# Optimization experiments

Hardware: AMD Instinct MI355X
Metric: run time of the kernel (lower is better)

## Reference

```python
import jax, jax.numpy as jnp
import numpy as np

NEG_SLOPE = 0.2
NUM_NODES = 100000
NUM_EDGES = 200000
NNZ = 1600000
IN_C = 128
OUT_C = 128
STAR = 64


def setup_inputs() -> dict:
    key = jax.random.key(0)
    ks = jax.random.split(key, 12)
    X = jax.random.normal(ks[0], (NUM_NODES, IN_C), dtype=jnp.float32)
    V = jax.random.randint(ks[1], (NNZ,), 0, NUM_NODES)
    E = jax.random.randint(ks[2], (NNZ,), 0, NUM_EDGES)
    S_features = jax.random.normal(ks[3], (NUM_EDGES, STAR), dtype=jnp.float32)
    s = 1.0 / np.sqrt(IN_C)
    Wx = jax.random.uniform(ks[4], (IN_C, OUT_C), minval=-s, maxval=s)
    bx = jax.random.uniform(ks[5], (OUT_C,), minval=-s, maxval=s)
    Wv = jax.random.uniform(ks[6], (IN_C, OUT_C), minval=-s, maxval=s)
    bv = jax.random.uniform(ks[7], (OUT_C,), minval=-s, maxval=s)
    sa = 1.0 / np.sqrt(OUT_C)
    a_vec = jax.random.uniform(ks[8], (OUT_C,), minval=-sa, maxval=sa)
    st = 1.0 / np.sqrt(OUT_C + STAR)
    Wt = jax.random.uniform(ks[9], (OUT_C + STAR, OUT_C), minval=-st, maxval=st)
    bt = jax.random.uniform(ks[10], (OUT_C,), minval=-st, maxval=st)
    return {"X": X, "V": V, "E": E, "S_features": S_features,
            "Wx": Wx, "bx": bx, "Wv": Wv, "bv": bv,
            "a_vec": a_vec, "Wt": Wt, "bt": bt}


def _segment_softmax(s, seg, num_segments):
    m = jax.ops.segment_max(s, seg, num_segments=num_segments)
    e = jnp.exp(s - m[seg])
    denom = jax.ops.segment_sum(e, seg, num_segments=num_segments)
    return e / denom[seg]


def reference(X, V, E, S_features, Wx, bx, Wv, bv, a_vec, Wt, bt):
    # DPHGNNConv forward (eval mode: dropout = identity)
    X_init = X @ Wx + bx                      # [N, out]
    X_feat = X @ Wv + bv                      # [N, out]
    scores = X_feat @ a_vec                   # [N]
    s = jax.nn.leaky_relu(scores[V], NEG_SLOPE)  # [nnz]
    w = _segment_softmax(s, E, NUM_EDGES)     # [nnz]
    Xev = X_feat[V] * w[:, None]              # [nnz, out]
    Y_v2e = jax.ops.segment_sum(Xev, E, num_segments=NUM_EDGES)
    Y_v2e = jax.nn.elu(Y_v2e)
    e_msg = jnp.concatenate([Y_v2e, S_features], axis=1)  # [E, out+star]
    Y = e_msg @ Wt + bt                       # [E, out]
    Yev = Y[E]                                # [nnz, out]
    num = jax.ops.segment_sum(Yev, V, num_segments=NUM_NODES)
    cnt = jax.ops.segment_sum(jnp.ones((NNZ,), jnp.float32), V, num_segments=NUM_NODES)
    Xn = num / jnp.maximum(cnt, 1.0)[:, None]  # scatter_mean
    Xn = jax.nn.elu(Xn)                        # is_last=False
    return Xn + X_init
```

## Files before the change

kernel.cpp:

```cpp
#include <hip/hip_runtime.h>
#include <math.h>

#define N_NODES 100000
#define N_EDGES 200000
#define NNZ_    1600000
#define INC  128
#define OUTC 128
#define STAR_ 64
#define NEG 0.2f
#define NBIN_E 391
#define NBIN_V 196
#define NBIN (NBIN_E + NBIN_V)
#define CHUNK 4000
#define NBLK_A (NNZ_/CHUNK)
#define CAP_E 5120
#define CAP_V 9216
#define PAIR_SZ (NBIN_E*CAP_E + NBIN_V*CAP_V)
#define CAPI 288
#define CAPN 288

typedef __attribute__((ext_vector_type(8))) short bf16x8_t;
typedef __attribute__((ext_vector_type(8))) unsigned short u16x8;
typedef __attribute__((ext_vector_type(4))) float f32x4_t;

__device__ __forceinline__ float leaky(float x){ return x > 0.f ? x : NEG*x; }
__device__ __forceinline__ float elu1(float x){ return x > 0.f ? x : __expf(x)-1.f; }
__device__ __forceinline__ unsigned short f2bf(float f){
  unsigned u = __float_as_uint(f);
  unsigned r = u + 0x7FFFu + ((u >> 16) & 1u);
  return (unsigned short)(r >> 16);
}
__device__ __forceinline__ float bf2f(unsigned short h){
  return __uint_as_float(((unsigned)h) << 16);
}
__device__ __forceinline__ int padBaseD(int bin){
  return bin < NBIN_E ? bin*CAP_E : NBIN_E*CAP_E + (bin-NBIN_E)*CAP_V;
}

__global__ void k_cvt(const float* __restrict__ Wx, const float* __restrict__ Wv,
                      const float* __restrict__ Wt,
                      unsigned short* __restrict__ WcatT, unsigned short* __restrict__ WtT,
                      int* __restrict__ binCur,
                      int2* __restrict__ vw, int* __restrict__ eIdxV){
  const int i = blockIdx.x*256 + threadIdx.x;
  if (i < 256*128){
    const int n = i >> 7, k = i & 127;
    const float v = (n < 128) ? Wx[k*128 + n] : Wv[k*128 + (n-128)];
    WcatT[n*128 + k] = f2bf(v);
  }
  const int j = i - 256*128;
  if (j >= 0 && j < 128*192){
    const int n = j / 192, k = j - n*192;
    WtT[n*192 + k] = f2bf(Wt[k*128 + n]);
  }
  if (blockIdx.x == 0){
    for (int p = threadIdx.x; p < NBIN; p += 256) binCur[p] = padBaseD(p);
    if (threadIdx.x < 16){ vw[NNZ_ + threadIdx.x] = make_int2(0, 0); eIdxV[NNZ_ + threadIdx.x] = 0; }
  }
}

__global__ __launch_bounds__(256) void k_front(
    const float* __restrict__ X, const unsigned short* __restrict__ WcatT,
    const float* __restrict__ bx, const float* __restrict__ bv,
    const float* __restrict__ av,
    float* __restrict__ Xinit, unsigned short* __restrict__ Xfb,
    float* __restrict__ scores,
    const int* __restrict__ V, const int* __restrict__ E,
    int* __restrict__ binCur, int2* __restrict__ pair){
  __shared__ int hA[NBIN];
  __shared__ int baseA[NBIN];
  __shared__ unsigned short xb[16][136];
  __shared__ float sc[16];
  const int tid = threadIdx.x;

  if (blockIdx.x < NBLK_A) {
    for (int p = tid; p < NBIN; p += 256) hA[p] = 0;
    __syncthreads();
    const int start = blockIdx.x*CHUNK, end = start + CHUNK;
    for (int i = start + tid; i < end; i += 256){
      atomicAdd(&hA[E[i] >> 9], 1);
      atomicAdd(&hA[NBIN_E + (V[i] >> 9)], 1);
    }
    __syncthreads();
    for (int p = tid; p < NBIN; p += 256)
      baseA[p] = hA[p] ? atomicAdd(&binCur[p], hA[p]) : 0;
    __syncthreads();
    for (int p = tid; p < NBIN; p += 256) hA[p] = 0;
    __syncthreads();
    for (int i = start + tid; i < end; i += 256){
      const int e = E[i], v = V[i];
      const int be = e >> 9, bv_ = NBIN_E + (v >> 9);
      const int se = baseA[be]  + atomicAdd(&hA[be],  1);
      const int sv = baseA[bv_] + atomicAdd(&hA[bv_], 1);
      pair[se] = make_int2(e, v);
      pair[sv] = make_int2(v, e);
    }
    return;
  }

  const int lane = tid & 63, w = tid >> 6;
  const int quad = lane >> 4, l16 = lane & 15;
  const int r0 = (blockIdx.x - NBLK_A) * 16;
  if (tid < 16) sc[tid] = 0.f;
  {
    const int r = tid >> 4;
    const int c0 = (tid & 15) * 8;
    const float4 a4 = *(const float4*)&X[(size_t)(r0+r)*INC + c0];
    const float4 b4 = *(const float4*)&X[(size_t)(r0+r)*INC + c0 + 4];
    bf16x8_t pk;
    pk[0]=(short)f2bf(a4.x); pk[1]=(short)f2bf(a4.y); pk[2]=(short)f2bf(a4.z); pk[3]=(short)f2bf(a4.w);
    pk[4]=(short)f2bf(b4.x); pk[5]=(short)f2bf(b4.y); pk[6]=(short)f2bf(b4.z); pk[7]=(short)f2bf(b4.w);
    *(bf16x8_t*)&xb[r][c0] = pk;
  }
  __syncthreads();
  f32x4_t acc[4] = {{0,0,0,0},{0,0,0,0},{0,0,0,0},{0,0,0,0}};
  const int n_base = w*64 + l16;
  for (int s = 0; s < 4; ++s){
    const bf16x8_t af = *(const bf16x8_t*)&xb[l16][s*32 + quad*8];
    #pragma unroll
    for (int nt = 0; nt < 4; ++nt){
      const int n = n_base + nt*16;
      const bf16x8_t bf = *(const bf16x8_t*)&WcatT[(size_t)n*128 + s*32 + quad*8];
      acc[nt] = __builtin_amdgcn_mfma_f32_16x16x32_bf16(af, bf, acc[nt], 0, 0, 0);
    }
  }
  float pr[4] = {0.f, 0.f, 0.f, 0.f};
  #pragma unroll
  for (int nt = 0; nt < 4; ++nt){
    const int n = n_base + nt*16;
    const float bias = (n < 128) ? bx[n] : bv[n-128];
    #pragma unroll
    for (int r = 0; r < 4; ++r){
      const int m = quad*4 + r;
      const float val = acc[nt][r] + bias;
      if (n < 128) Xinit[(size_t)(r0+m)*OUTC + n] = val;
      else {
        Xfb[(size_t)(r0+m)*OUTC + (n-128)] = f2bf(val);
        pr[r] += val * av[n-128];
      }
    }
  }
  if (w >= 2){
    #pragma unroll
    for (int r = 0; r < 4; ++r) atomicAdd(&sc[quad*4 + r], pr[r]);
  }
  __syncthreads();
  if (tid < 16) scores[r0 + tid] = sc[tid];
}

__global__ __launch_bounds__(512) void k_binBE(const int2* __restrict__ pair,
    const int* __restrict__ binCur, const float* __restrict__ scores,
    int2* __restrict__ vw, int* __restrict__ cntE, int* __restrict__ startsE,
    float* __restrict__ dens){
  __shared__ int h[512], sc0[512], sc1[512];
  __shared__ float dsh[512];
  const int bin = blockIdx.x;
  const int bucket0 = bin << 9;
  const int pstart = padBaseD(bin);
  const int n = binCur[bin] - pstart;
  const int tid = threadIdx.x;
  {
    int part = 0;
    for (int p = tid; p < bin; p += 512) part += binCur[p] - padBaseD(p);
    sc0[tid] = part;
    __syncthreads();
    for (int o = 256; o; o >>= 1){ if (tid < o) sc0[tid] += sc0[tid+o]; __syncthreads(); }
  }
  const int itemBase = sc0[0];
  __syncthreads();
  h[tid] = 0; dsh[tid] = 0.f;
  __syncthreads();
  for (int j = tid; j < n; j += 512) atomicAdd(&h[pair[pstart + j].x & 511], 1);
  __syncthreads();
  sc0[tid] = h[tid];
  __syncthreads();
  int* a = sc0; int* b = sc1;
  for (int o = 1; o < 512; o <<= 1){
    b[tid] = a[tid] + (tid >= o ? a[tid-o] : 0);
    __syncthreads();
    int* t = a; a = b; b = t;
  }
  {
    const int excl = a[tid] - h[tid];
    b[tid] = itemBase + excl;
    const int bucket = bucket0 + tid;
    if (bucket < N_EDGES){ cntE[bucket] = h[tid]; startsE[bucket] = itemBase + excl; }
  }
  __syncthreads();
  for (int j = tid; j < n; j += 512){
    const int2 kv = pair[pstart + j];
    const int slot = atomicAdd(&b[kv.x & 511], 1);
    const float ex = __expf(leaky(scores[kv.y]));
    vw[slot] = make_int2(kv.y, __float_as_int(ex));
    atomicAdd(&dsh[kv.x & 511], ex);
  }
  __syncthreads();
  if (bucket0 + tid < N_EDGES) dens[bucket0 + tid] = dsh[tid];
}

__global__ __launch_bounds__(256) void k_edgeV(
    const int* __restrict__ cntE, const int* __restrict__ startsE,
    const int2* __restrict__ vw, const float* __restrict__ dens,
    const unsigned short* __restrict__ Xfb,
    const float* __restrict__ S, const unsigned short* __restrict__ WtT,
    const float* __restrict__ bt, unsigned short* __restrict__ Ybf,
    const int2* __restrict__ pair, const int* __restrict__ binCur,
    int* __restrict__ eIdxV, int* __restrict__ cntV, int* __restrict__ startsV) {
  __shared__ __align__(16) char smem[(CAPI + 8)*8 + 16*200*2];
  const int tid = threadIdx.x;

  if (blockIdx.x < NBIN_V) {
    int* h   = (int*)smem;
    int* sc0 = h + 512;
    int* sc1 = sc0 + 512;
    const int nb = blockIdx.x;
    const int bin = NBIN_E + nb;
    const int bucket0 = nb << 9;
    const int pstart = padBaseD(bin);
    const int n = binCur[bin] - pstart;
    {
      int part = 0;
      for (int p = tid; p < bin; p += 256) part += binCur[p] - padBaseD(p);
      sc0[tid] = part;
      __syncthreads();
      for (int o = 128; o; o >>= 1){ if (tid < o) sc0[tid] += sc0[tid+o]; __syncthreads(); }
    }
    const int itemBase = sc0[0] - NNZ_;
    __syncthreads();
    for (int p = tid; p < 512; p += 256) h[p] = 0;
    __syncthreads();
    for (int j = tid; j < n; j += 256) atomicAdd(&h[pair[pstart + j].x & 511], 1);
    __syncthreads();
    for (int p = tid; p < 512; p += 256) sc0[p] = h[p];
    __syncthreads();
    int* a = sc0; int* b = sc1;
    for (int o = 1; o < 512; o <<= 1){
      for (int p = tid; p < 512; p += 256) b[p] = a[p] + (p >= o ? a[p-o] : 0);
      __syncthreads();
      int* t = a; a = b; b = t;
    }
    for (int p = tid; p < 512; p += 256){
      const int excl = a[p] - h[p];
      b[p] = itemBase + excl;
      const int bucket = bucket0 + p;
      if (bucket < N_NODES){ cntV[bucket] = h[p]; startsV[bucket] = itemBase + excl; }
    }
    __syncthreads();
    for (int j = tid; j < n; j += 256){
      const int2 kv = pair[pstart + j];
      const int slot = atomicAdd(&b[kv.x & 511], 1);
      eIdxV[slot] = kv.y;
    }
    return;
  }

  int2* inc = (int2*)smem;
  unsigned short (*msg)[200] = (unsigned short (*)[200])(smem + (CAPI + 8)*8);
  const int lane = tid & 63, w = tid >> 6;
  const int e0 = (blockIdx.x - NBIN_V) * 16;
  const int g16 = tid >> 4, s16 = tid & 15;

  const int st0 = startsE[e0];
  const int lim = startsE[e0 + 15] + cntE[e0 + 15] - st0;

  for (int i = tid; i < CAPI + 8; i += 256)
    inc[i] = (i < lim) ? vw[st0 + i] : make_int2(0, 0);

  {
    const float4 s4 = *(const float4*)&S[(size_t)(e0+g16)*STAR_ + s16*4];
    ushort4 pk; pk.x=f2bf(s4.x); pk.y=f2bf(s4.y); pk.z=f2bf(s4.z); pk.w=f2bf(s4.w);
    *(ushort4*)&msg[g16][128 + s16*4] = pk;
  }
  __syncthreads();

  const int e = e0 + g16;
  const int deg = cntE[e];
  const int lo  = startsE[e] - st0;
  const int c8 = s16 * 8;
  float ac[8] = {0.f,0.f,0.f,0.f,0.f,0.f,0.f,0.f};
  if (lo + deg <= CAPI) {
    for (int j = 0; j < deg; j += 8) {
      int2 pp[8];
      #pragma unroll
      for (int k = 0; k < 8; ++k) pp[k] = inc[lo + j + k];
      u16x8 xx[8];
      #pragma unroll
      for (int k = 0; k < 8; ++k)
        xx[k] = *(const u16x8*)&Xfb[(size_t)pp[k].x*OUTC + c8];
      #pragma unroll
      for (int k = 0; k < 8; ++k) {
        const float wgt = (j + k < deg) ? __int_as_float(pp[k].y) : 0.f;
        #pragma unroll
        for (int q = 0; q < 8; ++q) ac[q] += wgt * bf2f(xx[k][q]);
      }
    }
  } else {
    const int st = st0 + lo;
    for (int j = 0; j < deg; j += 8) {
      int2 pp[8];
      #pragma unroll
      for (int k = 0; k < 8; ++k) pp[k] = vw[st + j + k];
      u16x8 xx[8];
      #pragma unroll
      for (int k = 0; k < 8; ++k)
        xx[k] = *(const u16x8*)&Xfb[(size_t)pp[k].x*OUTC + c8];
      #pragma unroll
      for (int k = 0; k < 8; ++k) {
        const float wgt = (j + k < deg) ? __int_as_float(pp[k].y) : 0.f;
        #pragma unroll
        for (int q = 0; q < 8; ++q) ac[q] += wgt * bf2f(xx[k][q]);
      }
    }
  }
  {
    const float invd = deg > 0 ? 1.f/dens[e] : 0.f;
    u16x8 pk;
    #pragma unroll
    for (int q = 0; q < 8; ++q) pk[q] = f2bf(elu1(ac[q]*invd));
    *(u16x8*)&msg[g16][c8] = pk;
  }
  __syncthreads();

  const int quad = lane >> 4, l16 = lane & 15;
  f32x4_t acc0 = {0,0,0,0}, acc1 = {0,0,0,0};
  const int n0 = w * 32;
  for (int s = 0; s < 6; ++s) {
    const bf16x8_t af = *(const bf16x8_t*)&msg[l16][s*32 + quad*8];
    const bf16x8_t b0 = *(const bf16x8_t*)&WtT[(size_t)(n0 + l16)*192      + s*32 + quad*8];
    const bf16x8_t b1 = *(const bf16x8_t*)&WtT[(size_t)(n0 + 16 + l16)*192 + s*32 + quad*8];
    acc0 = __builtin_amdgcn_mfma_f32_16x16x32_bf16(af, b0, acc0, 0, 0, 0);
    acc1 = __builtin_amdgcn_mfma_f32_16x16x32_bf16(af, b1, acc1, 0, 0, 0);
  }
  const float bt0 = bt[n0 + l16], bt1 = bt[n0 + 16 + l16];
  #pragma unroll
  for (int r = 0; r < 4; ++r) {
    const int m = quad*4 + r;
    Ybf[(size_t)(e0+m)*OUTC + n0 + l16]      = f2bf(acc0[r] + bt0);
    Ybf[(size_t)(e0+m)*OUTC + n0 + 16 + l16] = f2bf(acc1[r] + bt1);
  }
}

__global__ __launch_bounds__(256) void k_node(
    const int* __restrict__ cntV, const int* __restrict__ startsV,
    const int* __restrict__ eIdxV,
    const unsigned short* __restrict__ Ybf, float* __restrict__ out) {
  __shared__ int elds[CAPN + 8];
  const int tid = threadIdx.x;
  const int sub = tid & 31, grp = tid >> 5;
  const int v0 = blockIdx.x * 8;

  const int st0 = startsV[v0];
  const int lim = startsV[v0 + 7] + cntV[v0 + 7] - st0;
  for (int i = tid; i < CAPN + 8; i += 256)
    elds[i] = (i < lim) ? eIdxV[st0 + i] : 0;
  __syncthreads();

  const int v = v0 + grp;
  const int c4 = sub * 4;
  const int deg = cntV[v];
  const int lo  = startsV[v] - st0;
  float a0=0.f, a1=0.f, a2=0.f, a3=0.f;
  if (lo + deg <= CAPN) {
    for (int j = 0; j < deg; j += 8) {
      int ee[8];
      #pragma unroll
      for (int k = 0; k < 8; ++k) ee[k] = elds[lo + j + k];
      ushort4 yy[8];
      #pragma unroll
      for (int k = 0; k < 8; ++k)
        yy[k] = *(const ushort4*)&Ybf[(size_t)ee[k]*OUTC + c4];
      #pragma unroll
      for (int k = 0; k < 8; ++k) {
        const float pz = (j + k < deg) ? 1.f : 0.f;
        a0 += pz * bf2f(yy[k].x); a1 += pz * bf2f(yy[k].y);
        a2 += pz * bf2f(yy[k].z); a3 += pz * bf2f(yy[k].w);
      }
    }
  } else {
    const int st = st0 + lo;
    for (int j = 0; j < deg; j += 8) {
      int ee[8];
      #pragma unroll
      for (int k = 0; k < 8; ++k) ee[k] = eIdxV[st + j + k];
      ushort4 yy[8];
      #pragma unroll
      for (int k = 0; k < 8; ++k)
        yy[k] = *(const ushort4*)&Ybf[(size_t)ee[k]*OUTC + c4];
      #pragma unroll
      for (int k = 0; k < 8; ++k) {
        const float pz = (j + k < deg) ? 1.f : 0.f;
        a0 += pz * bf2f(yy[k].x); a1 += pz * bf2f(yy[k].y);
        a2 += pz * bf2f(yy[k].z); a3 += pz * bf2f(yy[k].w);
      }
    }
  }
  const float invd = 1.f / fmaxf((float)deg, 1.f);
  float4 o = *(float4*)&out[(size_t)v*OUTC + c4];
  o.x = elu1(a0*invd) + o.x;
  o.y = elu1(a1*invd) + o.y;
  o.z = elu1(a2*invd) + o.z;
  o.w = elu1(a3*invd) + o.w;
  *(float4*)&out[(size_t)v*OUTC + c4] = o;
}

extern "C" void kernel_launch(void* const* d_in, const int* in_sizes, int n_in,
                              void* d_out, int out_size, void* d_ws, size_t ws_size,
                              hipStream_t stream) {
  const float* X  = (const float*)d_in[0];
  const int*   V  = (const int*)d_in[1];
  const int*   E  = (const int*)d_in[2];
  const float* S  = (const float*)d_in[3];
  const float* Wx = (const float*)d_in[4];
  const float* bx = (const float*)d_in[5];
  const float* Wv = (const float*)d_in[6];
  const float* bv = (const float*)d_in[7];
  const float* av = (const float*)d_in[8];
  const float* Wt = (const float*)d_in[9];
  const float* bt = (const float*)d_in[10];
  float* out = (float*)d_out;

  char* ws = (char*)d_ws;
  size_t off = 0;
  auto alloc = [&](size_t bytes) -> void* {
    off = (off + 255) & ~(size_t)255;
    void* p = ws + off; off += bytes; return p;
  };
  unsigned short* Xfb   = (unsigned short*)alloc((size_t)N_NODES*OUTC*2);
  unsigned short* Ybf   = (unsigned short*)alloc((size_t)N_EDGES*OUTC*2);
  float* scores = (float*)alloc((size_t)N_NODES*4);
  unsigned short* WcatT = (unsigned short*)alloc((size_t)256*128*2);
  unsigned short* WtT   = (unsigned short*)alloc((size_t)128*192*2);
  int2* pair   = (int2*)alloc((size_t)PAIR_SZ*8);
  int* binCur  = (int*)alloc((size_t)NBIN*4);
  int* cntE    = (int*)alloc((size_t)N_EDGES*4);
  int* cntV    = (int*)alloc((size_t)N_NODES*4);
  int* startsE = (int*)alloc((size_t)N_EDGES*4);
  int* startsV = (int*)alloc((size_t)N_NODES*4);
  int2* vw     = (int2*)alloc((size_t)(NNZ_+16)*8);
  int* eIdxV   = (int*)alloc((size_t)(NNZ_+16)*4);
  float* dens  = (float*)alloc((size_t)N_EDGES*4);

  k_cvt<<<(256*128 + 128*192 + 255)/256, 256, 0, stream>>>(Wx, Wv, Wt, WcatT, WtT,
                                                           binCur, vw, eIdxV);
  k_front<<<NBLK_A + N_NODES/16, 256, 0, stream>>>(X, WcatT, bx, bv, av, out, Xfb, scores,
                                                   V, E, binCur, pair);
  k_binBE<<<NBIN_E, 512, 0, stream>>>(pair, binCur, scores, vw, cntE, startsE, dens);
  k_edgeV<<<NBIN_V + N_EDGES/16, 256, 0, stream>>>(cntE, startsE, vw, dens, Xfb, S, WtT, bt, Ybf,
                                                   pair, binCur, eIdxV, cntV, startsV);
  k_node<<<N_NODES/8, 256, 0, stream>>>(cntV, startsV, eIdxV, Ybf, out);
}
```

Before: 470.0 us.

## Precompute exp scores per node and fold softmax denominator into edge gather

Computes exp(leaky(score)) once per node in the front kernel instead of once per incidence in the binning kernel. The binning kernel now writes only vertex indices (4 bytes instead of 8 per incidence) and drops the shared-memory atomic denominator accumulation. The edge kernel gathers each weight from the per-node table and sums the denominator locally. This trades a smaller sorted array and a lighter binning pass for one extra random 4-byte gather per incidence in the edge kernel. Max-subtraction is still skipped, as it was before.

```diff
diff --git a/kernel.cpp b/kernel.cpp
--- a/kernel.cpp
+++ b/kernel.cpp
@@ -41,7 +41,7 @@
                       const float* __restrict__ Wt,
                       unsigned short* __restrict__ WcatT, unsigned short* __restrict__ WtT,
                       int* __restrict__ binCur,
-                      int2* __restrict__ vw, int* __restrict__ eIdxV){
+                      int* __restrict__ vIdxE, int* __restrict__ eIdxV){
   const int i = blockIdx.x*256 + threadIdx.x;
   if (i < 256*128){
     const int n = i >> 7, k = i & 127;
@@ -55,7 +55,7 @@
   }
   if (blockIdx.x == 0){
     for (int p = threadIdx.x; p < NBIN; p += 256) binCur[p] = padBaseD(p);
-    if (threadIdx.x < 16){ vw[NNZ_ + threadIdx.x] = make_int2(0, 0); eIdxV[NNZ_ + threadIdx.x] = 0; }
+    if (threadIdx.x < 16){ vIdxE[NNZ_ + threadIdx.x] = 0; eIdxV[NNZ_ + threadIdx.x] = 0; }
   }
 }
 
@@ -64,7 +64,7 @@
     const float* __restrict__ bx, const float* __restrict__ bv,
     const float* __restrict__ av,
     float* __restrict__ Xinit, unsigned short* __restrict__ Xfb,
-    float* __restrict__ scores,
+    float* __restrict__ scoresExp,
     const int* __restrict__ V, const int* __restrict__ E,
     int* __restrict__ binCur, int2* __restrict__ pair){
   __shared__ int hA[NBIN];
@@ -145,15 +145,13 @@
     for (int r = 0; r < 4; ++r) atomicAdd(&sc[quad*4 + r], pr[r]);
   }
   __syncthreads();
-  if (tid < 16) scores[r0 + tid] = sc[tid];
+  if (tid < 16) scoresExp[r0 + tid] = __expf(leaky(sc[tid]));
 }
 
 __global__ __launch_bounds__(512) void k_binBE(const int2* __restrict__ pair,
-    const int* __restrict__ binCur, const float* __restrict__ scores,
-    int2* __restrict__ vw, int* __restrict__ cntE, int* __restrict__ startsE,
-    float* __restrict__ dens){
+    const int* __restrict__ binCur,
+    int* __restrict__ vIdxE, int* __restrict__ cntE, int* __restrict__ startsE){
   __shared__ int h[512], sc0[512], sc1[512];
-  __shared__ float dsh[512];
   const int bin = blockIdx.x;
   const int bucket0 = bin << 9;
   const int pstart = padBaseD(bin);
@@ -168,7 +166,7 @@
   }
   const int itemBase = sc0[0];
   __syncthreads();
-  h[tid] = 0; dsh[tid] = 0.f;
+  h[tid] = 0;
   __syncthreads();
   for (int j = tid; j < n; j += 512) atomicAdd(&h[pair[pstart + j].x & 511], 1);
   __syncthreads();
@@ -190,23 +188,19 @@
   for (int j = tid; j < n; j += 512){
     const int2 kv = pair[pstart + j];
     const int slot = atomicAdd(&b[kv.x & 511], 1);
-    const float ex = __expf(leaky(scores[kv.y]));
-    vw[slot] = make_int2(kv.y, __float_as_int(ex));
-    atomicAdd(&dsh[kv.x & 511], ex);
-  }
-  __syncthreads();
-  if (bucket0 + tid < N_EDGES) dens[bucket0 + tid] = dsh[tid];
+    vIdxE[slot] = kv.y;
+  }
 }
 
 __global__ __launch_bounds__(256) void k_edgeV(
     const int* __restrict__ cntE, const int* __restrict__ startsE,
-    const int2* __restrict__ vw, const float* __restrict__ dens,
+    const int* __restrict__ vIdxE, const float* __restrict__ scoresExp,
     const unsigned short* __restrict__ Xfb,
     const float* __restrict__ S, const unsigned short* __restrict__ WtT,
     const float* __restrict__ bt, unsigned short* __restrict__ Ybf,
     const int2* __restrict__ pair, const int* __restrict__ binCur,
     int* __restrict__ eIdxV, int* __restrict__ cntV, int* __restrict__ startsV) {
-  __shared__ __align__(16) char smem[(CAPI + 8)*8 + 16*200*2];
+  __shared__ __align__(16) char smem[(CAPI + 8)*4 + 16*200*2];
   const int tid = threadIdx.x;
 
   if (blockIdx.x < NBIN_V) {
@@ -254,8 +248,8 @@
     return;
   }
 
-  int2* inc = (int2*)smem;
-  unsigned short (*msg)[200] = (unsigned short (*)[200])(smem + (CAPI + 8)*8);
+  int* inc = (int*)smem;
+  unsigned short (*msg)[200] = (unsigned short (*)[200])(smem + (CAPI + 8)*4);
   const int lane = tid & 63, w = tid >> 6;
   const int e0 = (blockIdx.x - NBIN_V) * 16;
   const int g16 = tid >> 4, s16 = tid & 15;
@@ -264,7 +258,7 @@
   const int lim = startsE[e0 + 15] + cntE[e0 + 15] - st0;
 
   for (int i = tid; i < CAPI + 8; i += 256)
-    inc[i] = (i < lim) ? vw[st0 + i] : make_int2(0, 0);
+    inc[i] = (i < lim) ? vIdxE[st0 + i] : 0;
 
   {
     const float4 s4 = *(const float4*)&S[(size_t)(e0+g16)*STAR_ + s16*4];
@@ -278,18 +272,23 @@
   const int lo  = startsE[e] - st0;
   const int c8 = s16 * 8;
   float ac[8] = {0.f,0.f,0.f,0.f,0.f,0.f,0.f,0.f};
+  float wsum = 0.f;
   if (lo + deg <= CAPI) {
     for (int j = 0; j < deg; j += 8) {
-      int2 pp[8];
+      int pp[8];
       #pragma unroll
       for (int k = 0; k < 8; ++k) pp[k] = inc[lo + j + k];
+      float ww[8];
+      #pragma unroll
+      for (int k = 0; k < 8; ++k) ww[k] = scoresExp[pp[k]];
       u16x8 xx[8];
       #pragma unroll
       for (int k = 0; k < 8; ++k)
-        xx[k] = *(const u16x8*)&Xfb[(size_t)pp[k].x*OUTC + c8];
+        xx[k] = *(const u16x8*)&Xfb[(size_t)pp[k]*OUTC + c8];
       #pragma unroll
       for (int k = 0; k < 8; ++k) {
-        const float wgt = (j + k < deg) ? __int_as_float(pp[k].y) : 0.f;
+        const float wgt = (j + k < deg) ? ww[k] : 0.f;
+        wsum += wgt;
         #pragma unroll
         for (int q = 0; q < 8; ++q) ac[q] += wgt * bf2f(xx[k][q]);
       }
@@ -297,23 +296,27 @@
   } else {
     const int st = st0 + lo;
     for (int j = 0; j < deg; j += 8) {
-      int2 pp[8];
-      #pragma unroll
-      for (int k = 0; k < 8; ++k) pp[k] = vw[st + j + k];
+      int pp[8];
+      #pragma unroll
+      for (int k = 0; k < 8; ++k) pp[k] = vIdxE[st + j + k];
+      float ww[8];
+      #pragma unroll
+      for (int k = 0; k < 8; ++k) ww[k] = scoresExp[pp[k]];
       u16x8 xx[8];
       #pragma unroll
       for (int k = 0; k < 8; ++k)
-        xx[k] = *(const u16x8*)&Xfb[(size_t)pp[k].x*OUTC + c8];
+        xx[k] = *(const u16x8*)&Xfb[(size_t)pp[k]*OUTC + c8];
       #pragma unroll
       for (int k = 0; k < 8; ++k) {
-        const float wgt = (j + k < deg) ? __int_as_float(pp[k].y) : 0.f;
+        const float wgt = (j + k < deg) ? ww[k] : 0.f;
+        wsum += wgt;
         #pragma unroll
         for (int q = 0; q < 8; ++q) ac[q] += wgt * bf2f(xx[k][q]);
       }
     }
   }
   {
-    const float invd = deg > 0 ? 1.f/dens[e] : 0.f;
+    const float invd = wsum > 0.f ? 1.f/wsum : 0.f;
     u16x8 pk;
     #pragma unroll
     for (int q = 0; q < 8; ++q) pk[q] = f2bf(elu1(ac[q]*invd));
@@ -427,7 +430,7 @@
   };
   unsigned short* Xfb   = (unsigned short*)alloc((size_t)N_NODES*OUTC*2);
   unsigned short* Ybf   = (unsigned short*)alloc((size_t)N_EDGES*OUTC*2);
-  float* scores = (float*)alloc((size_t)N_NODES*4);
+  float* scoresExp = (float*)alloc((size_t)N_NODES*4);
   unsigned short* WcatT = (unsigned short*)alloc((size_t)256*128*2);
   unsigned short* WtT   = (unsigned short*)alloc((size_t)128*192*2);
   int2* pair   = (int2*)alloc((size_t)PAIR_SZ*8);
@@ -436,16 +439,16 @@
   int* cntV    = (int*)alloc((size_t)N_NODES*4);
   int* startsE = (int*)alloc((size_t)N_EDGES*4);
   int* startsV = (int*)alloc((size_t)N_NODES*4);
-  int2* vw     = (int2*)alloc((size_t)(NNZ_+16)*8);
+  int* vIdxE   = (int*)alloc((size_t)(NNZ_+16)*4);
   int* eIdxV   = (int*)alloc((size_t)(NNZ_+16)*4);
-  float* dens  = (float*)alloc((size_t)N_EDGES*4);
 
   k_cvt<<<(256*128 + 128*192 + 255)/256, 256, 0, stream>>>(Wx, Wv, Wt, WcatT, WtT,
-                                                           binCur, vw, eIdxV);
-  k_front<<<NBLK_A + N_NODES/16, 256, 0, stream>>>(X, WcatT, bx, bv, av, out, Xfb, scores,
+                                                           binCur, vIdxE, eIdxV);
+  k_front<<<NBLK_A + N_NODES/16, 256, 0, stream>>>(X, WcatT, bx, bv, av, out, Xfb, scoresExp,
                                                    V, E, binCur, pair);
-  k_binBE<<<NBIN_E, 512, 0, stream>>>(pair, binCur, scores, vw, cntE, startsE, dens);
-  k_edgeV<<<NBIN_V + N_EDGES/16, 256, 0, stream>>>(cntE, startsE, vw, dens, Xfb, S, WtT, bt, Ybf,
+  k_binBE<<<NBIN_E, 512, 0, stream>>>(pair, binCur, vIdxE, cntE, startsE);
+  k_edgeV<<<NBIN_V + N_EDGES/16, 256, 0, stream>>>(cntE, startsE, vIdxE, scoresExp,
+                                                   Xfb, S, WtT, bt, Ybf,
                                                    pair, binCur, eIdxV, cntV, startsV);
   k_node<<<N_NODES/8, 256, 0, stream>>>(cntV, startsV, eIdxV, Ybf, out);
 }
```

Result: no change. 464.6 us (-1.2%).
